# Optimization experiments

Hardware: AMD Instinct MI355X
Metric: run time of the kernel (lower is better)

## Reference

```python
import jax, jax.numpy as jnp
import numpy as np

EMBED_DIM = 1024
NUM_HEADS = 8
HEAD_DIM = EMBED_DIM // NUM_HEADS
EARLY_BIAS = 2.0


def setup_inputs() -> dict:
    key = jax.random.key(0)
    ks = jax.random.split(key, 8)
    B, T, C = 32, 2048, EMBED_DIM
    s = 0.02
    return {
        "x": jax.random.normal(ks[0], (B, T, C), dtype=jnp.float32),
        "mask": jnp.ones((B, T), dtype=jnp.int32),
        "query_token": jax.random.normal(ks[1], (C,), dtype=jnp.float32),
        "kv_w": jax.random.normal(ks[2], (2 * C, C), dtype=jnp.float32) * s,
        "kv_b": jnp.zeros((2 * C,), dtype=jnp.float32),
        "q_w": jax.random.normal(ks[3], (C, C), dtype=jnp.float32) * s,
        "q_b": jnp.zeros((C,), dtype=jnp.float32),
        "proj_w": jax.random.normal(ks[4], (C, C), dtype=jnp.float32) * s,
        "proj_b": jnp.zeros((C,), dtype=jnp.float32),
    }


def reference(x, mask, query_token, kv_w, kv_b, q_w, q_b, proj_w, proj_b):
    B, T, C = x.shape
    H, D = NUM_HEADS, HEAD_DIM
    scale = D ** -0.5
    # kv projection: [B,T,2C] -> split into k,v of [B,T,H,D]
    kv = x @ kv_w.T + kv_b
    kv = kv.reshape(B, T, 2, H, D)
    k, v = kv[:, :, 0], kv[:, :, 1]
    # single learned query (shared across batch): [H,D]
    q = (query_token @ q_w.T + q_b).reshape(H, D)
    # scores: [B,H,T]
    attn = jnp.einsum('hd,bthd->bht', q, k) * scale
    # early-segment exponential-decay temporal bias: [T]
    pos = jnp.arange(T, dtype=x.dtype)
    bias = EARLY_BIAS * jnp.exp(-pos / (T / 3.0))
    attn = attn + bias[None, None, :]
    attn = jnp.where(mask[:, None, :] == 0, -jnp.inf, attn)
    attn = jax.nn.softmax(attn, axis=-1)  # dropout is identity in eval
    # weighted sum over time: [B,H,D] -> [B,C]
    pooled = jnp.einsum('bht,bthd->bhd', attn, v).reshape(B, C)
    pooled = pooled @ proj_w.T + proj_b
    attn_weights = attn.mean(axis=1)  # [B,T]
    return pooled, attn_weights
```

## Files before the change

### kernel.cpp

```cpp
#include <hip/hip_runtime.h>
#include <math.h>

#define NB 32
#define NT 2048
#define NC 1024
#define NH 8
#define ND 128
#define TCH 16
#define SCALE_F 0.08838834764831845f

template <int CTRL>
__device__ __forceinline__ float dppadd(float x) {
  int t = __builtin_amdgcn_update_dpp(0, __float_as_int(x), CTRL, 0xf, 0xf, true);
  return x + __int_as_float(t);
}
__device__ __forceinline__ float wredsum(float v) {
  v = dppadd<0x111>(v);
  v = dppadd<0x112>(v);
  v = dppadd<0x114>(v);
  v = dppadd<0x118>(v);
  v = dppadd<0x142>(v);
  v = dppadd<0x143>(v);
  return __int_as_float(__builtin_amdgcn_readlane(__float_as_int(v), 63));
}

__device__ __forceinline__ void barx() {
  asm volatile("s_waitcnt lgkmcnt(0)" ::: "memory");
  __builtin_amdgcn_s_barrier();
  asm volatile("" ::: "memory");
}

__global__ __launch_bounds__(256) void k_wqp(const float* __restrict__ qt,
                                             const float* __restrict__ q_w,
                                             const float* __restrict__ q_b,
                                             const float* __restrict__ kv_w,
                                             float* __restrict__ qout,
                                             float* __restrict__ wqp) {
  __shared__ float qs[16];
  int h = blockIdx.x >> 3, dq = blockIdx.x & 7;
  int tid = threadIdx.x;
  int dbase = h * ND + dq * 16;
  {
    int row = tid >> 4;
    int cg = tid & 15;
    const float4* qw4 = (const float4*)(q_w + (size_t)(dbase + row) * NC);
    const float4* qt4 = (const float4*)qt;
    float p = 0.f;
#pragma unroll 8
    for (int j = 0; j < 16; ++j) {
      float4 wv = qw4[j * 16 + cg];
      float4 av = qt4[j * 16 + cg];
      p += av.x * wv.x + av.y * wv.y + av.z * wv.z + av.w * wv.w;
    }
    p += __shfl_xor(p, 1, 64);
    p += __shfl_xor(p, 2, 64);
    p += __shfl_xor(p, 4, 64);
    p += __shfl_xor(p, 8, 64);
    if (cg == 0) qs[row] = p + q_b[dbase + row];
  }
  __syncthreads();
  if (tid < 16) qout[dbase + tid] = qs[tid];
  const float4* kw4 = (const float4*)kv_w;
  float4 acc = make_float4(0.f, 0.f, 0.f, 0.f);
#pragma unroll 8
  for (int dd = 0; dd < 16; ++dd) {
    float qv = qs[dd];
    float4 kv = kw4[(size_t)(dbase + dd) * 256 + tid];
    acc.x = fmaf(qv, kv.x, acc.x); acc.y = fmaf(qv, kv.y, acc.y);
    acc.z = fmaf(qv, kv.z, acc.z); acc.w = fmaf(qv, kv.w, acc.w);
  }
  ((float4*)wqp)[dq * 2048 + h * 256 + tid] = acc;
}

__global__ __launch_bounds__(256, 2) void k_fused(
    const float* __restrict__ x, const int* __restrict__ mask,
    const float* __restrict__ wqp, const float* __restrict__ q,
    const float* __restrict__ kv_b,
    float* __restrict__ S, float* __restrict__ partAcc,
    float* __restrict__ partML) {
  __shared__ float4 xs4[2 * 512];
  int bi = blockIdx.x;
  int b = bi >> 4;
  int tc = bi & (TCH - 1);
  int tid = threadIdx.x;
  int w = tid >> 6, lane = tid & 63;
  int h0 = w * 2;
  int tbase = tc * 128;

  const float4* wqp4 = (const float4*)wqp;
  float4 wqv[2][4];
#pragma unroll
  for (int hh = 0; hh < 2; ++hh)
#pragma unroll
    for (int j = 0; j < 4; ++j) {
      int idx = (h0 + hh) * 256 + lane + 64 * j;
      float sx = 0.f, sy = 0.f, sz = 0.f, sw = 0.f;
#pragma unroll
      for (int p = 0; p < 8; ++p) {
        float4 t = wqp4[p * 2048 + idx];
        sx += t.x; sy += t.y; sz += t.z; sw += t.w;
      }
      wqv[hh][j] = make_float4(sx, sy, sz, sw);
    }
  float qkbv[2];
#pragma unroll
  for (int hh = 0; hh < 2; ++hh) {
    float p = 0.f;
    if (lane < 32) {
      float4 qv = ((const float4*)(q + (h0 + hh) * ND))[lane];
      float4 bv = ((const float4*)(kv_b + (h0 + hh) * ND))[lane];
      p = qv.x * bv.x + qv.y * bv.y + qv.z * bv.z + qv.w * bv.w;
    }
    qkbv[hh] = wredsum(p);
  }
  unsigned long long bm0 = __ballot(mask[b * NT + tbase + lane] != 0);
  unsigned long long bm1 = __ballot(mask[b * NT + tbase + 64 + lane] != 0);

  float m[2] = {-INFINITY, -INFINITY};
  float l[2] = {0.f, 0.f};
  float4 acc[2][4];
#pragma unroll
  for (int hh = 0; hh < 2; ++hh)
#pragma unroll
    for (int j = 0; j < 4; ++j) acc[hh][j] = make_float4(0.f, 0.f, 0.f, 0.f);
  float sreg[2][2] = {{0.f, 0.f}, {0.f, 0.f}};

  const float4* x4 = (const float4*)(x + (size_t)(b * NT + tbase) * NC);

  {
    float4 s0 = x4[tid], s1 = x4[256 + tid];
    xs4[tid] = s0;
    xs4[256 + tid] = s1;
  }
  barx();
  float4 pa0 = x4[2 * 256 + tid], pa1 = x4[3 * 256 + tid];
  float4 pb0 = x4[4 * 256 + tid], pb1 = x4[5 * 256 + tid];

#define COMPUTE_STEP(STEP, SLOT)                                               \
  {                                                                            \
    int t0 = tbase + (STEP) * 2;                                               \
    unsigned long long bmx = ((STEP) < 32) ? bm0 : bm1;                        \
    int sh = (2 * (STEP)) & 63;                                                \
    int mk0 = (int)((bmx >> (unsigned)sh) & 1ull);                             \
    int mk1 = (int)((bmx >> (unsigned)(sh + 1)) & 1ull);                       \
    float bias0 = 2.0f * __expf((float)t0 * (-3.0f / 2048.0f));                \
    float bias1 = 2.0f * __expf((float)(t0 + 1) * (-3.0f / 2048.0f));          \
    float4 xv[2][4];                                                           \
    _Pragma("unroll") for (int r = 0; r < 2; ++r)                              \
        _Pragma("unroll") for (int j = 0; j < 4; ++j)                          \
            xv[r][j] = xs4[(SLOT) * 512 + r * 256 + lane + 64 * j];            \
    _Pragma("unroll") for (int hh = 0; hh < 2; ++hh) {                         \
      float d0 = 0.f, d1 = 0.f;                                                \
      _Pragma("unroll") for (int j = 0; j < 4; ++j) {                          \
        float4 wv = wqv[hh][j];                                                \
        d0 = fmaf(xv[0][j].x, wv.x, d0); d0 = fmaf(xv[0][j].y, wv.y, d0);      \
        d0 = fmaf(xv[0][j].z, wv.z, d0); d0 = fmaf(xv[0][j].w, wv.w, d0);      \
        d1 = fmaf(xv[1][j].x, wv.x, d1); d1 = fmaf(xv[1][j].y, wv.y, d1);      \
        d1 = fmaf(xv[1][j].z, wv.z, d1); d1 = fmaf(xv[1][j].w, wv.w, d1);      \
      }                                                                        \
      d0 = wredsum(d0);                                                        \
      d1 = wredsum(d1);                                                        \
      float v0 = mk0 ? (d0 + qkbv[hh]) * SCALE_F + bias0 : -INFINITY;          \
      float v1 = mk1 ? (d1 + qkbv[hh]) * SCALE_F + bias1 : -INFINITY;          \
      sreg[hh][0] = (lane == (STEP)) ? v0 : sreg[hh][0];                       \
      sreg[hh][1] = (lane == (STEP)) ? v1 : sreg[hh][1];                       \
      float pmax = fmaxf(v0, v1);                                              \
      if (pmax > m[hh] + 8.0f) {                  \
        float r = __expf(m[hh] - pmax);                                        \
        l[hh] *= r;                                                            \
        _Pragma("unroll") for (int j = 0; j < 4; ++j) {                        \
          acc[hh][j].x *= r; acc[hh][j].y *= r;                                \
          acc[hh][j].z *= r; acc[hh][j].w *= r;                                \
        }                                                                      \
        m[hh] = pmax;                                                          \
      }                                                                        \
      float p0 = mk0 ? __expf(v0 - m[hh]) : 0.f;                               \
      float p1 = mk1 ? __expf(v1 - m[hh]) : 0.f;                               \
      l[hh] += p0 + p1;                                                        \
      _Pragma("unroll") for (int j = 0; j < 4; ++j) {                          \
        acc[hh][j].x = fmaf(p0, xv[0][j].x, fmaf(p1, xv[1][j].x, acc[hh][j].x)); \
        acc[hh][j].y = fmaf(p0, xv[0][j].y, fmaf(p1, xv[1][j].y, acc[hh][j].y)); \
        acc[hh][j].z = fmaf(p0, xv[0][j].z, fmaf(p1, xv[1][j].z, acc[hh][j].z)); \
        acc[hh][j].w = fmaf(p0, xv[0][j].w, fmaf(p1, xv[1][j].w, acc[hh][j].w)); \
      }                                                                        \
    }                                                                          \
  }

  for (int k = 0; k < 32; ++k) {
    COMPUTE_STEP(2 * k, 0)
    xs4[512 + tid] = pa0;
    xs4[512 + 256 + tid] = pa1;
    if (k < 31) {
      pa0 = x4[(4 * k + 6) * 256 + tid];
      pa1 = x4[(4 * k + 7) * 256 + tid];
    }
    barx();
    COMPUTE_STEP(2 * k + 1, 1)
    if (k < 31) {
      xs4[tid] = pb0;
      xs4[256 + tid] = pb1;
      if (k < 30) {
        pb0 = x4[(4 * k + 8) * 256 + tid];
        pb1 = x4[(4 * k + 9) * 256 + tid];
      }
      barx();
    }
  }
#undef COMPUTE_STEP

#pragma unroll
  for (int hh = 0; hh < 2; ++hh) {
    float2 sv = make_float2(sreg[hh][0], sreg[hh][1]);
    float2* sp = (float2*)(S + ((size_t)(b * NH + h0 + hh)) * NT + tbase);
    sp[lane] = sv;
  }
  float4* pA = (float4*)(partAcc + (size_t)bi * (NH * NC));
#pragma unroll
  for (int hh = 0; hh < 2; ++hh)
#pragma unroll
    for (int j = 0; j < 4; ++j)
      pA[(h0 + hh) * 256 + lane + 64 * j] = acc[hh][j];
  if (lane == 0) {
#pragma unroll
    for (int hh = 0; hh < 2; ++hh) {
      partML[(bi * NH + h0 + hh) * 2] = m[hh];
      partML[(bi * NH + h0 + hh) * 2 + 1] = l[hh];
    }
  }
}

__global__ __launch_bounds__(256) void k_xaw(const float* __restrict__ partAcc,
                                             const float* __restrict__ partML,
                                             const float* __restrict__ S,
                                             float* __restrict__ xa,
                                             float* __restrict__ ow) {
  __shared__ float Ms[NH], Is[NH];
  int blk = blockIdx.x;
  int tid = threadIdx.x;
  if (blk < NB * NH) {
    int b = blk >> 3, h = blk & 7;
    float mv = -INFINITY, lv = 0.f;
    if (tid < TCH) {
      mv = partML[((b * TCH + tid) * NH + h) * 2];
      lv = partML[((b * TCH + tid) * NH + h) * 2 + 1];
    }
    float Mg = mv;
#pragma unroll
    for (int off = 8; off > 0; off >>= 1) Mg = fmaxf(Mg, __shfl_xor(Mg, off, 64));
    float contrib = (tid < TCH && mv != -INFINITY) ? __expf(mv - Mg) * lv : 0.f;
#pragma unroll
    for (int off = 8; off > 0; off >>= 1) contrib += __shfl_xor(contrib, off, 64);
    if (tid == 0) {
      Ms[0] = Mg;
      Is[0] = (contrib > 0.f) ? 1.f / contrib : 0.f;
    }
    __syncthreads();
    float Mgb = Ms[0], inv = Is[0];
    float4 sacc = make_float4(0.f, 0.f, 0.f, 0.f);
    for (int tc = 0; tc < TCH; ++tc) {
      int pi = (b * TCH + tc) * NH + h;
      float mw = partML[pi * 2];
      if (mw == -INFINITY) continue;
      float scl = __expf(mw - Mgb);
      float4 v = ((const float4*)partAcc)[(size_t)pi * 256 + tid];
      sacc.x = fmaf(scl, v.x, sacc.x); sacc.y = fmaf(scl, v.y, sacc.y);
      sacc.z = fmaf(scl, v.z, sacc.z); sacc.w = fmaf(scl, v.w, sacc.w);
    }
    sacc.x *= inv; sacc.y *= inv; sacc.z *= inv; sacc.w *= inv;
    ((float4*)xa)[(size_t)blk * 256 + tid] = sacc;
  } else {
    int blkb = blk - NB * NH;
    int b = blkb >> 3, tch = blkb & 7;
    int hh = tid >> 4, tcc = tid & 15;
    float mv = -INFINITY, lv = 0.f;
    if (tid < 128) {
      mv = partML[((b * TCH + tcc) * NH + hh) * 2];
      lv = partML[((b * TCH + tcc) * NH + hh) * 2 + 1];
    }
    float Mg = mv;
#pragma unroll
    for (int off = 8; off > 0; off >>= 1) Mg = fmaxf(Mg, __shfl_xor(Mg, off, 64));
    float contrib = (tid < 128 && mv != -INFINITY) ? __expf(mv - Mg) * lv : 0.f;
#pragma unroll
    for (int off = 8; off > 0; off >>= 1) contrib += __shfl_xor(contrib, off, 64);
    if (tid < 128 && tcc == 0) {
      Ms[hh] = Mg;
      Is[hh] = (contrib > 0.f) ? 1.f / contrib : 0.f;
    }
    __syncthreads();
    int t = tch * 256 + tid;
    float a = 0.f;
#pragma unroll
    for (int h = 0; h < NH; ++h) {
      float s = S[((size_t)(b * NH + h)) * NT + t];
      a += (s == -INFINITY) ? 0.f : __expf(s - Ms[h]) * Is[h];
    }
    ow[(size_t)b * NT + t] = a * 0.125f;
  }
}

__global__ __launch_bounds__(256) void k_pv(const float* __restrict__ xa,
                                            const float* __restrict__ kv_w,
                                            const float* __restrict__ kv_b,
                                            float* __restrict__ p2) {
  int gw = (blockIdx.x * 256 + threadIdx.x) >> 6;
  int lane = threadIdx.x & 63;
  int hd = gw & (NC - 1);
  int bg = gw >> 10;
  int h = hd >> 7;
  const float4* w4 = (const float4*)(kv_w + ((size_t)(NC + hd)) * NC);
  float4 wv[4];
#pragma unroll
  for (int j = 0; j < 4; ++j) wv[j] = w4[lane + 64 * j];
  float accv[4] = {0.f, 0.f, 0.f, 0.f};
#pragma unroll
  for (int i = 0; i < 4; ++i) {
    const float4* a4 =
        (const float4*)(xa + ((size_t)((bg * 4 + i) * NH + h)) * NC);
#pragma unroll
    for (int j = 0; j < 4; ++j) {
      float4 a = a4[lane + 64 * j];
      accv[i] += a.x * wv[j].x + a.y * wv[j].y + a.z * wv[j].z + a.w * wv[j].w;
    }
  }
#pragma unroll
  for (int i = 0; i < 4; ++i) accv[i] = wredsum(accv[i]);
  if (lane == 0) {
    float bias = kv_b[NC + hd];
#pragma unroll
    for (int i = 0; i < 4; ++i)
      p2[(size_t)(bg * 4 + i) * NC + hd] = accv[i] + bias;
  }
}

__global__ __launch_bounds__(256) void k_proj(const float* __restrict__ p2,
                                              const float* __restrict__ proj_w,
                                              const float* __restrict__ proj_b,
                                              float* __restrict__ out) {
  int gw = (blockIdx.x * 256 + threadIdx.x) >> 6;
  int lane = threadIdx.x & 63;
  int i = gw & (NC - 1);
  int bg = gw >> 10;
  const float4* w4 = (const float4*)(proj_w + (size_t)i * NC);
  float4 wv[4];
#pragma unroll
  for (int j = 0; j < 4; ++j) wv[j] = w4[lane + 64 * j];
  float accv[4] = {0.f, 0.f, 0.f, 0.f};
#pragma unroll
  for (int k = 0; k < 4; ++k) {
    const float4* a4 = (const float4*)(p2 + (size_t)(bg * 4 + k) * NC);
#pragma unroll
    for (int j = 0; j < 4; ++j) {
      float4 a = a4[lane + 64 * j];
      accv[k] += a.x * wv[j].x + a.y * wv[j].y + a.z * wv[j].z + a.w * wv[j].w;
    }
  }
#pragma unroll
  for (int k = 0; k < 4; ++k) accv[k] = wredsum(accv[k]);
  if (lane == 0) {
    float bias = proj_b[i];
#pragma unroll
    for (int k = 0; k < 4; ++k)
      out[(size_t)(bg * 4 + k) * NC + i] = accv[k] + bias;
  }
}

extern "C" void kernel_launch(void* const* d_in, const int* in_sizes, int n_in,
                              void* d_out, int out_size, void* d_ws, size_t ws_size,
                              hipStream_t stream) {
  const float* x = (const float*)d_in[0];
  const int* mask = (const int*)d_in[1];
  const float* qt = (const float*)d_in[2];
  const float* kv_w = (const float*)d_in[3];
  const float* kv_b = (const float*)d_in[4];
  const float* q_w = (const float*)d_in[5];
  const float* q_b = (const float*)d_in[6];
  const float* proj_w = (const float*)d_in[7];
  const float* proj_b = (const float*)d_in[8];
  float* out = (float*)d_out;

  float* ws = (float*)d_ws;
  float* q = ws;
  float* wqp = ws + 1024;
  float* S = ws + 66560;
  float* partAcc = ws + 590848;
  float* partML = ws + 4785152;
  float* xa = ws + 4793344;
  float* p2 = ws + 5055488;

  k_wqp<<<64, 256, 0, stream>>>(qt, q_w, q_b, kv_w, q, wqp);
  k_fused<<<NB * TCH, 256, 0, stream>>>(x, mask, wqp, q, kv_b, S, partAcc, partML);
  k_xaw<<<512, 256, 0, stream>>>(partAcc, partML, S, xa, out + NB * NC);
  k_pv<<<2048, 256, 0, stream>>>(xa, kv_w, kv_b, p2);
  k_proj<<<2048, 256, 0, stream>>>(p2, proj_w, proj_b, out);
}
```

Measured before the change: 105.0 us.

## Replace LDS-staged x tiles with per-wave register double-buffered global loads

Drops the shared-memory ping-pong buffer and its block barriers in the fused attention-pooling kernel. Each wave now loads its two x rows straight from global memory into two register buffers, fetching the next step while computing the current one. This removes LDS traffic and synchronisation. The cost is that all four waves in a block read the same x rows, giving 4x redundant global/L2 requests, and the extra register buffers raise VGPR pressure.

```diff
diff --git a/kernel.cpp b/kernel.cpp
--- a/kernel.cpp
+++ b/kernel.cpp
@@ -22,12 +22,6 @@
   v = dppadd<0x142>(v);
   v = dppadd<0x143>(v);
   return __int_as_float(__builtin_amdgcn_readlane(__float_as_int(v), 63));
-}
-
-__device__ __forceinline__ void barx() {
-  asm volatile("s_waitcnt lgkmcnt(0)" ::: "memory");
-  __builtin_amdgcn_s_barrier();
-  asm volatile("" ::: "memory");
 }
 
 __global__ __launch_bounds__(256) void k_wqp(const float* __restrict__ qt,
@@ -78,7 +72,6 @@
     const float* __restrict__ kv_b,
     float* __restrict__ S, float* __restrict__ partAcc,
     float* __restrict__ partML) {
-  __shared__ float4 xs4[2 * 512];
   int bi = blockIdx.x;
   int b = bi >> 4;
   int tc = bi & (TCH - 1);
@@ -127,16 +120,20 @@
 
   const float4* x4 = (const float4*)(x + (size_t)(b * NT + tbase) * NC);
 
-  {
-    float4 s0 = x4[tid], s1 = x4[256 + tid];
-    xs4[tid] = s0;
-    xs4[256 + tid] = s1;
-  }
-  barx();
-  float4 pa0 = x4[2 * 256 + tid], pa1 = x4[3 * 256 + tid];
-  float4 pb0 = x4[4 * 256 + tid], pb1 = x4[5 * 256 + tid];
-
-#define COMPUTE_STEP(STEP, SLOT)                                               \
+  float4 xvA[2][4], xvB[2][4];
+#pragma unroll
+  for (int r = 0; r < 2; ++r)
+#pragma unroll
+    for (int j = 0; j < 4; ++j) xvA[r][j] = x4[r * 256 + lane + 64 * j];
+
+#define ISSUE(BUF, STEP)                                                       \
+  {                                                                            \
+    _Pragma("unroll") for (int r = 0; r < 2; ++r)                              \
+        _Pragma("unroll") for (int j = 0; j < 4; ++j)                          \
+            BUF[r][j] = x4[((STEP) * 2 + r) * 256 + lane + 64 * j];            \
+  }
+
+#define COMPUTE_STEP(STEP, BUF)                                                \
   {                                                                            \
     int t0 = tbase + (STEP) * 2;                                               \
     unsigned long long bmx = ((STEP) < 32) ? bm0 : bm1;                        \
@@ -145,18 +142,14 @@
     int mk1 = (int)((bmx >> (unsigned)(sh + 1)) & 1ull);                       \
     float bias0 = 2.0f * __expf((float)t0 * (-3.0f / 2048.0f));                \
     float bias1 = 2.0f * __expf((float)(t0 + 1) * (-3.0f / 2048.0f));          \
-    float4 xv[2][4];                                                           \
-    _Pragma("unroll") for (int r = 0; r < 2; ++r)                              \
-        _Pragma("unroll") for (int j = 0; j < 4; ++j)                          \
-            xv[r][j] = xs4[(SLOT) * 512 + r * 256 + lane + 64 * j];            \
     _Pragma("unroll") for (int hh = 0; hh < 2; ++hh) {                         \
       float d0 = 0.f, d1 = 0.f;                                                \
       _Pragma("unroll") for (int j = 0; j < 4; ++j) {                          \
         float4 wv = wqv[hh][j];                                                \
-        d0 = fmaf(xv[0][j].x, wv.x, d0); d0 = fmaf(xv[0][j].y, wv.y, d0);      \
-        d0 = fmaf(xv[0][j].z, wv.z, d0); d0 = fmaf(xv[0][j].w, wv.w, d0);      \
-        d1 = fmaf(xv[1][j].x, wv.x, d1); d1 = fmaf(xv[1][j].y, wv.y, d1);      \
-        d1 = fmaf(xv[1][j].z, wv.z, d1); d1 = fmaf(xv[1][j].w, wv.w, d1);      \
+        d0 = fmaf(BUF[0][j].x, wv.x, d0); d0 = fmaf(BUF[0][j].y, wv.y, d0);    \
+        d0 = fmaf(BUF[0][j].z, wv.z, d0); d0 = fmaf(BUF[0][j].w, wv.w, d0);    \
+        d1 = fmaf(BUF[1][j].x, wv.x, d1); d1 = fmaf(BUF[1][j].y, wv.y, d1);    \
+        d1 = fmaf(BUF[1][j].z, wv.z, d1); d1 = fmaf(BUF[1][j].w, wv.w, d1);    \
       }                                                                        \
       d0 = wredsum(d0);                                                        \
       d1 = wredsum(d1);                                                        \
@@ -178,35 +171,22 @@
       float p1 = mk1 ? __expf(v1 - m[hh]) : 0.f;                               \
       l[hh] += p0 + p1;                                                        \
       _Pragma("unroll") for (int j = 0; j < 4; ++j) {                          \
-        acc[hh][j].x = fmaf(p0, xv[0][j].x, fmaf(p1, xv[1][j].x, acc[hh][j].x)); \
-        acc[hh][j].y = fmaf(p0, xv[0][j].y, fmaf(p1, xv[1][j].y, acc[hh][j].y)); \
-        acc[hh][j].z = fmaf(p0, xv[0][j].z, fmaf(p1, xv[1][j].z, acc[hh][j].z)); \
-        acc[hh][j].w = fmaf(p0, xv[0][j].w, fmaf(p1, xv[1][j].w, acc[hh][j].w)); \
+        acc[hh][j].x = fmaf(p0, BUF[0][j].x, fmaf(p1, BUF[1][j].x, acc[hh][j].x)); \
+        acc[hh][j].y = fmaf(p0, BUF[0][j].y, fmaf(p1, BUF[1][j].y, acc[hh][j].y)); \
+        acc[hh][j].z = fmaf(p0, BUF[0][j].z, fmaf(p1, BUF[1][j].z, acc[hh][j].z)); \
+        acc[hh][j].w = fmaf(p0, BUF[0][j].w, fmaf(p1, BUF[1][j].w, acc[hh][j].w)); \
       }                                                                        \
     }                                                                          \
   }
 
   for (int k = 0; k < 32; ++k) {
-    COMPUTE_STEP(2 * k, 0)
-    xs4[512 + tid] = pa0;
-    xs4[512 + 256 + tid] = pa1;
-    if (k < 31) {
-      pa0 = x4[(4 * k + 6) * 256 + tid];
-      pa1 = x4[(4 * k + 7) * 256 + tid];
-    }
-    barx();
-    COMPUTE_STEP(2 * k + 1, 1)
-    if (k < 31) {
-      xs4[tid] = pb0;
-      xs4[256 + tid] = pb1;
-      if (k < 30) {
-        pb0 = x4[(4 * k + 8) * 256 + tid];
-        pb1 = x4[(4 * k + 9) * 256 + tid];
-      }
-      barx();
-    }
+    if (k > 0 || true) { ISSUE(xvB, 2 * k + 1) }
+    COMPUTE_STEP(2 * k, xvA)
+    if (k < 31) { ISSUE(xvA, 2 * k + 2) }
+    COMPUTE_STEP(2 * k + 1, xvB)
   }
 #undef COMPUTE_STEP
+#undef ISSUE
 
 #pragma unroll
   for (int hh = 0; hh < 2; ++hh) {
```

After: 113.5 us. +8.1%, slower.
